# Kernel tuning notes

Hardware: AMD Instinct MI355X
Metric: run time of the kernel (lower is better)

## Reference

```python
import jax, jax.numpy as jnp
import numpy as np
from jax import lax

N_NODES = 50000
N_EDGES = 1_600_000
BATCH = 4
T_STEPS = 50
DT = 0.02  # integration step (s)


def setup_inputs() -> dict:
    key = jax.random.key(0)
    ks = jax.random.split(key, 8)
    x = jax.random.normal(ks[0], (BATCH, T_STEPS, N_NODES), jnp.float32) * 0.5
    # NeuronBias: normal(mean=0.5, std=0.05)
    bias = (jax.random.normal(ks[1], (N_NODES,), jnp.float32) * 0.05 + 0.5)
    # NeuronTimeConst: around 0.05s, kept positive
    time_const = jax.random.uniform(ks[2], (N_NODES,), jnp.float32) * 0.045 + 0.005
    # EdgeSign: +/-1
    sign = jnp.where(jax.random.uniform(ks[3], (N_EDGES,)) < 0.5, -1.0, 1.0).astype(jnp.float32)
    # SynCount: lognormal, non-negative
    syn_count = jnp.exp(jax.random.normal(ks[4], (N_EDGES,), jnp.float32) * 0.5)
    # SynStrength: small positive scale (scale_chem/scale_elec = 0.01)
    syn_strength = jax.random.uniform(ks[5], (N_EDGES,), jnp.float32) * 0.01
    src_idx = jax.random.randint(ks[6], (N_EDGES,), 0, N_NODES, dtype=jnp.int32)
    tgt_idx = jax.random.randint(ks[7], (N_EDGES,), 0, N_NODES, dtype=jnp.int32)
    return dict(x=x, bias=bias, time_const=time_const, sign=sign,
                syn_count=syn_count, syn_strength=syn_strength,
                src_idx=src_idx, tgt_idx=tgt_idx)


def reference(x, bias, time_const, sign, syn_count, syn_strength, src_idx, tgt_idx):
    """Recurrent connectome dynamics (StaticSynapses, relu activation).

    Per step: gather relu(v) at source nodes, weight each edge by
    sign*syn_count*syn_strength, scatter-add into target nodes, then Euler
    update v += dt/tau * (-v + bias + synaptic_input + stimulus).
    Returns relu(v) over time: [B, T, N].
    """
    B, T, N = x.shape
    # clamp configs: non_negative on counts/strengths
    weight = sign * jax.nn.relu(syn_count) * jax.nn.relu(syn_strength)  # [E]
    tau = jnp.maximum(time_const, DT)
    alpha = DT / tau  # [N]

    v0 = jnp.broadcast_to(bias, (B, N))  # initial state at bias

    def step(v, x_t):
        rates = jax.nn.relu(v)                      # [B, N]
        msg = rates[:, src_idx] * weight            # gather -> edge transform [B, E]
        summed = jnp.zeros((B, N), x.dtype).at[:, tgt_idx].add(msg)  # scatter-reduce
        v_new = v + alpha * (-v + bias + summed + x_t)
        return v_new, jax.nn.relu(v_new)

    _, out = lax.scan(step, v0, jnp.moveaxis(x, 1, 0))  # scan over T
    return jnp.moveaxis(out, 0, 1)  # [B, T, N]
```

## Files before the change

### kernel.cpp

```cpp
#include <hip/hip_runtime.h>
#include <hip/hip_fp16.h>

#define N_NODES 50000
#define N_EDGES 1600000
#define T_STEPS 50
#define DT      0.02f
#define NB      256
#define NPB     196
#define CAP     6912
#define TILE    4096
#define G       8


__global__ __launch_bounds__(256) void zero_kernel(int* __restrict__ bucket_count) {
    bucket_count[threadIdx.x] = 0;
}

__global__ __launch_bounds__(256) void init_kernel(
    const float* __restrict__ bias, const float* __restrict__ time_const,
    float* __restrict__ alpha, float* __restrict__ v ,
    float4* __restrict__ rates0)
{
    int n = blockIdx.x * 256 + threadIdx.x;
    if (n >= N_NODES) return;
    float tau = fmaxf(time_const[n], DT);
    alpha[n] = DT / tau;
    float b = bias[n];
    v[n] = b; v[N_NODES + n] = b; v[2 * N_NODES + n] = b; v[3 * N_NODES + n] = b;
    float r = fmaxf(b, 0.0f);
    rates0[n] = make_float4(r, r, r, r);
}

__global__ __launch_bounds__(256) void bucket_kernel(
    const int* __restrict__ src, const int* __restrict__ tgt,
    const float* __restrict__ sign, const float* __restrict__ syn_count,
    const float* __restrict__ syn_strength,
    int* __restrict__ bucket_count, unsigned long long* __restrict__ rec_buf)
{
    __shared__ int hist[NB], base_s[NB], cur[NB];
    int tid = threadIdx.x;
    hist[tid] = 0;
    __syncthreads();

    int e0 = blockIdx.x * TILE + tid;
    int bkt[16];
    unsigned long long item[16];
#pragma unroll
    for (int k = 0; k < 16; ++k) {
        int e = e0 + k * 256;
        if (e < N_EDGES) {
            int t = tgt[e];
            int b = t / NPB;
            int tl = t - b * NPB;
            float w = sign[e] * fmaxf(syn_count[e], 0.f) * fmaxf(syn_strength[e], 0.f);
            unsigned int rec = (unsigned int)src[e] |
                               ((unsigned int)__half_as_ushort(__float2half(w)) << 16);
            bkt[k] = b;
            item[k] = (unsigned long long)rec | ((unsigned long long)tl << 32);
            atomicAdd(&hist[b], 1);
        } else {
            bkt[k] = -1;
        }
    }
    __syncthreads();
    base_s[tid] = atomicAdd(&bucket_count[tid], hist[tid]);
    cur[tid] = 0;
    __syncthreads();
#pragma unroll
    for (int k = 0; k < 16; ++k) {
        if (bkt[k] >= 0) {
            int p = base_s[bkt[k]] + atomicAdd(&cur[bkt[k]], 1);
            if (p < CAP) rec_buf[(size_t)bkt[k] * CAP + p] = item[k];
        }
    }
}

__global__ __launch_bounds__(256) void sort_kernel(
    const int* __restrict__ bucket_count,
    const unsigned long long* __restrict__ rec_buf,
    unsigned int* __restrict__ edges_g, int* __restrict__ offsets)
{
    __shared__ unsigned int sorted[CAP];
    __shared__ int cnts[NB];
    __shared__ int loc_off[NPB + 1];
    __shared__ int loc_cur[NPB];

    int b = blockIdx.x;
    int tid = threadIdx.x;
    int node_base = b * NPB;
    int n_nodes = min(NPB, N_NODES - node_base);

    cnts[tid] = min(bucket_count[tid], CAP);
    if (tid < NPB) loc_cur[tid] = 0;
    __syncthreads();

    __shared__ int ebase_s;
    if (tid == 0) {
        int r = 0;
        for (int i = 0; i < b; ++i) r += cnts[i];
        ebase_s = r;
    }
    __syncthreads();
    int ebase = ebase_s;
    int cnt = cnts[b];

    for (int i = tid; i < cnt; i += 256) {
        unsigned long long it = rec_buf[(size_t)b * CAP + i];
        atomicAdd(&loc_cur[(int)(it >> 32)], 1);
    }
    __syncthreads();
    if (tid == 0) {
        int r = 0;
        for (int n = 0; n < n_nodes; ++n) { loc_off[n] = r; r += loc_cur[n]; }
        loc_off[n_nodes] = r;
    }
    __syncthreads();
    if (tid < n_nodes) loc_cur[tid] = loc_off[tid];
    __syncthreads();

    for (int i = tid; i < cnt; i += 256) {
        unsigned long long it = rec_buf[(size_t)b * CAP + i];
        int p = atomicAdd(&loc_cur[(int)(it >> 32)], 1);
        sorted[p] = (unsigned int)it;
    }
    __syncthreads();

    for (int i = tid; i < cnt; i += 256) edges_g[ebase + i] = sorted[i];
    for (int n = tid; n < n_nodes; n += 256) offsets[node_base + n] = ebase + loc_off[n];
    if (b == NB - 1 && tid == 0) offsets[N_NODES] = ebase + cnt;
}

__device__ __forceinline__ float rec_w(unsigned int rec) {
    return __half2float(__ushort_as_half((unsigned short)(rec >> 16)));
}

__global__ __launch_bounds__(256) void step_kernel(
    const float4* __restrict__ rates_in, float* __restrict__ rates_out,
    float* __restrict__ v ,
    const float* __restrict__ alpha, const float* __restrict__ bias,
    const int* __restrict__ offsets, const unsigned int* __restrict__ edges,
    const float* __restrict__ x, float* __restrict__ out, int t, int nblk)
{
    int nb8 = nblk / 8;
    int idx = blockIdx.x;
    int node_block = (idx < nb8 * 8) ? (idx % 8) * nb8 + idx / 8 : idx;
    int node = node_block * (256 / G) + ((int)threadIdx.x / G);
    int lane = threadIdx.x & (G - 1);
    if (node >= N_NODES) return;

    int beg = offsets[node], end = offsets[node + 1];
    float4 acc = make_float4(0.f, 0.f, 0.f, 0.f);

    int i = beg + lane;
    unsigned int r0 = (i          < end) ? edges[i]         : 0u;
    unsigned int r1 = (i + G      < end) ? edges[i + G]     : 0u;
    unsigned int r2 = (i + 2 * G  < end) ? edges[i + 2 * G] : 0u;
    unsigned int r3 = (i + 3 * G  < end) ? edges[i + 3 * G] : 0u;
    while (i < end) {
        unsigned int n0 = (i + 4 * G < end) ? edges[i + 4 * G] : 0u;
        unsigned int n1 = (i + 5 * G < end) ? edges[i + 5 * G] : 0u;
        unsigned int n2 = (i + 6 * G < end) ? edges[i + 6 * G] : 0u;
        unsigned int n3 = (i + 7 * G < end) ? edges[i + 7 * G] : 0u;
        float4 a0 = rates_in[r0 & 0xFFFFu];
        float4 a1 = rates_in[r1 & 0xFFFFu];
        float4 a2 = rates_in[r2 & 0xFFFFu];
        float4 a3 = rates_in[r3 & 0xFFFFu];
        float w0 = rec_w(r0), w1 = rec_w(r1), w2 = rec_w(r2), w3 = rec_w(r3);
        acc.x = fmaf(a0.x, w0, acc.x); acc.y = fmaf(a0.y, w0, acc.y);
        acc.z = fmaf(a0.z, w0, acc.z); acc.w = fmaf(a0.w, w0, acc.w);
        acc.x = fmaf(a1.x, w1, acc.x); acc.y = fmaf(a1.y, w1, acc.y);
        acc.z = fmaf(a1.z, w1, acc.z); acc.w = fmaf(a1.w, w1, acc.w);
        acc.x = fmaf(a2.x, w2, acc.x); acc.y = fmaf(a2.y, w2, acc.y);
        acc.z = fmaf(a2.z, w2, acc.z); acc.w = fmaf(a2.w, w2, acc.w);
        acc.x = fmaf(a3.x, w3, acc.x); acc.y = fmaf(a3.y, w3, acc.y);
        acc.z = fmaf(a3.z, w3, acc.z); acc.w = fmaf(a3.w, w3, acc.w);
        r0 = n0; r1 = n1; r2 = n2; r3 = n3;
        i += 4 * G;
    }

#pragma unroll
    for (int m = 1; m < G; m <<= 1) {
        acc.x += __shfl_xor(acc.x, m, 64);
        acc.y += __shfl_xor(acc.y, m, 64);
        acc.z += __shfl_xor(acc.z, m, 64);
        acc.w += __shfl_xor(acc.w, m, 64);
    }

    if (lane < 4) {
        float sum = (lane == 0) ? acc.x : (lane == 1) ? acc.y
                  : (lane == 2) ? acc.z : acc.w;
        float a = alpha[node];
        float b = bias[node];
        const int TN = T_STEPS * N_NODES;
        int vi = lane * N_NODES + node;
        int oi = lane * TN + t * N_NODES + node;
        float vv = v[vi];
        float vn = vv + a * (b + sum + x[oi] - vv);
        v[vi] = vn;
        float r = fmaxf(vn, 0.f);
        rates_out[node * 4 + lane] = r;
        out[oi] = r;
    }
}


extern "C" void kernel_launch(void* const* d_in, const int* in_sizes, int n_in,
                              void* d_out, int out_size, void* d_ws, size_t ws_size,
                              hipStream_t stream) {
    const float* x            = (const float*)d_in[0];
    const float* bias         = (const float*)d_in[1];
    const float* time_const   = (const float*)d_in[2];
    const float* sign         = (const float*)d_in[3];
    const float* syn_count    = (const float*)d_in[4];
    const float* syn_strength = (const float*)d_in[5];
    const int*   src_idx      = (const int*)d_in[6];
    const int*   tgt_idx      = (const int*)d_in[7];
    float* out = (float*)d_out;

    char* ws = (char*)d_ws;
    size_t off = 0;
    auto alloc = [&](size_t bytes) -> void* {
        void* p = ws + off;
        off = (off + bytes + 255) & ~(size_t)255;
        return p;
    };
    float* v        = (float*)alloc((size_t)N_NODES * 4 * 4);
    float* rates_a  = (float*)alloc((size_t)N_NODES * 16);
    float* rates_b  = (float*)alloc((size_t)N_NODES * 16);
    float* alpha    = (float*)alloc((size_t)N_NODES * 4);
    int*   offsets  = (int*)  alloc((size_t)(N_NODES + 1) * 4);
    int*   bucket_count = (int*)alloc((size_t)NB * 4);
    unsigned int* edges = (unsigned int*)alloc((size_t)N_EDGES * 4);
    unsigned long long* rec_buf =
        (unsigned long long*)alloc((size_t)NB * CAP * 8);

    int nb_nodes = (N_NODES + 255) / 256;
    int nb_tiles = (N_EDGES + TILE - 1) / TILE;

    zero_kernel<<<1, 256, 0, stream>>>(bucket_count);
    init_kernel<<<nb_nodes, 256, 0, stream>>>(bias, time_const, alpha, v,
                                              (float4*)rates_a);
    bucket_kernel<<<nb_tiles, 256, 0, stream>>>(src_idx, tgt_idx, sign, syn_count,
                                                syn_strength, bucket_count, rec_buf);
    sort_kernel<<<NB, 256, 0, stream>>>(bucket_count, rec_buf, edges, offsets);

    int nblk = (N_NODES + (256 / G) - 1) / (256 / G);
    for (int t = 0; t < T_STEPS; ++t) {
        const float4* rin  = (const float4*)((t & 1) ? rates_b : rates_a);
        float*        rout = (t & 1) ? rates_a : rates_b;
        step_kernel<<<nblk, 256, 0, stream>>>(rin, rout, v, alpha, bias,
                                              offsets, edges, x, out, t, nblk);
    }
}
```

Before: 735.8 us.

## Store rates in fp16, pad edge lists for paired loads, fuse init into sort

The per-node rate buffer is now stored as four fp16 values (8 bytes) instead of float4, which halves the bytes moved by each gathered edge read. Edge segments are padded to even length in fixed per-bucket slots, so each lane loads two edge records at once with a uint2 load. Explicit end offsets are stored per node. The init kernel is folded into the sort kernel, alpha and bias are packed into one float2, and nontemporal loads and stores are used for x and the output. Storing rates in fp16 adds rounding error to the recurrent state feeding each step.

```diff
diff --git a/kernel.cpp b/kernel.cpp
--- a/kernel.cpp
+++ b/kernel.cpp
@@ -8,27 +8,13 @@
 #define NB      256
 #define NPB     196
 #define CAP     6912
+#define CAP2    7168
 #define TILE    4096
 #define G       8
 
 
 __global__ __launch_bounds__(256) void zero_kernel(int* __restrict__ bucket_count) {
     bucket_count[threadIdx.x] = 0;
-}
-
-__global__ __launch_bounds__(256) void init_kernel(
-    const float* __restrict__ bias, const float* __restrict__ time_const,
-    float* __restrict__ alpha, float* __restrict__ v ,
-    float4* __restrict__ rates0)
-{
-    int n = blockIdx.x * 256 + threadIdx.x;
-    if (n >= N_NODES) return;
-    float tau = fmaxf(time_const[n], DT);
-    alpha[n] = DT / tau;
-    float b = bias[n];
-    v[n] = b; v[N_NODES + n] = b; v[2 * N_NODES + n] = b; v[3 * N_NODES + n] = b;
-    float r = fmaxf(b, 0.0f);
-    rates0[n] = make_float4(r, r, r, r);
 }
 
 __global__ __launch_bounds__(256) void bucket_kernel(
@@ -78,40 +64,39 @@
 __global__ __launch_bounds__(256) void sort_kernel(
     const int* __restrict__ bucket_count,
     const unsigned long long* __restrict__ rec_buf,
-    unsigned int* __restrict__ edges_g, int* __restrict__ offsets)
+    const float* __restrict__ bias, const float* __restrict__ time_const,
+    unsigned int* __restrict__ edges_g,
+    int* __restrict__ offsets, int* __restrict__ ends,
+    float2* __restrict__ ab, float* __restrict__ v ,
+    uint2* __restrict__ rates0 )
 {
-    __shared__ unsigned int sorted[CAP];
-    __shared__ int cnts[NB];
+    __shared__ unsigned int sorted[CAP2];
     __shared__ int loc_off[NPB + 1];
+    __shared__ int loc_cnt[NPB];
     __shared__ int loc_cur[NPB];
 
     int b = blockIdx.x;
     int tid = threadIdx.x;
     int node_base = b * NPB;
     int n_nodes = min(NPB, N_NODES - node_base);
-
-    cnts[tid] = min(bucket_count[tid], CAP);
-    if (tid < NPB) loc_cur[tid] = 0;
-    __syncthreads();
-
-    __shared__ int ebase_s;
+    int ebase = b * CAP2;
+    int cnt = min(bucket_count[b], CAP);
+
+    for (int i = tid; i < CAP2; i += 256) sorted[i] = 0;
+    if (tid < NPB) loc_cnt[tid] = 0;
+    __syncthreads();
+
+    for (int i = tid; i < cnt; i += 256) {
+        unsigned long long it = rec_buf[(size_t)b * CAP + i];
+        atomicAdd(&loc_cnt[(int)(it >> 32)], 1);
+    }
+    __syncthreads();
     if (tid == 0) {
         int r = 0;
-        for (int i = 0; i < b; ++i) r += cnts[i];
-        ebase_s = r;
-    }
-    __syncthreads();
-    int ebase = ebase_s;
-    int cnt = cnts[b];
-
-    for (int i = tid; i < cnt; i += 256) {
-        unsigned long long it = rec_buf[(size_t)b * CAP + i];
-        atomicAdd(&loc_cur[(int)(it >> 32)], 1);
-    }
-    __syncthreads();
-    if (tid == 0) {
-        int r = 0;
-        for (int n = 0; n < n_nodes; ++n) { loc_off[n] = r; r += loc_cur[n]; }
+        for (int n = 0; n < n_nodes; ++n) {
+            loc_off[n] = r;
+            r += (loc_cnt[n] + 1) & ~1;
+        }
         loc_off[n_nodes] = r;
     }
     __syncthreads();
@@ -125,20 +110,42 @@
     }
     __syncthreads();
 
-    for (int i = tid; i < cnt; i += 256) edges_g[ebase + i] = sorted[i];
-    for (int n = tid; n < n_nodes; n += 256) offsets[node_base + n] = ebase + loc_off[n];
-    if (b == NB - 1 && tid == 0) offsets[N_NODES] = ebase + cnt;
+    int total = loc_off[n_nodes];
+    for (int i = tid; i < total; i += 256) edges_g[ebase + i] = sorted[i];
+    for (int n = tid; n < n_nodes; n += 256) {
+        int gn = node_base + n;
+        offsets[gn] = ebase + loc_off[n];
+        ends[gn]    = ebase + loc_off[n + 1];
+        float bb  = bias[gn];
+        float tau = fmaxf(time_const[gn], DT);
+        ab[gn] = make_float2(DT / tau, bb);
+        v[gn] = bb; v[N_NODES + gn] = bb;
+        v[2 * N_NODES + gn] = bb; v[3 * N_NODES + gn] = bb;
+        __half hr = __float2half(fmaxf(bb, 0.f));
+        __half2 h2 = __halves2half2(hr, hr);
+        uint2 r0; r0.x = *(unsigned int*)&h2; r0.y = r0.x;
+        rates0[gn] = r0;
+    }
 }
 
 __device__ __forceinline__ float rec_w(unsigned int rec) {
     return __half2float(__ushort_as_half((unsigned short)(rec >> 16)));
 }
+__device__ __forceinline__ float4 h4_to_f4(uint2 g) {
+    __half2 h01 = *(__half2*)&g.x;
+    __half2 h23 = *(__half2*)&g.y;
+    float2 f01 = __half22float2(h01);
+    float2 f23 = __half22float2(h23);
+    return make_float4(f01.x, f01.y, f23.x, f23.y);
+}
 
 __global__ __launch_bounds__(256) void step_kernel(
-    const float4* __restrict__ rates_in, float* __restrict__ rates_out,
+    const uint2* __restrict__ rates_in ,
+    __half* __restrict__ rates_out ,
     float* __restrict__ v ,
-    const float* __restrict__ alpha, const float* __restrict__ bias,
-    const int* __restrict__ offsets, const unsigned int* __restrict__ edges,
+    const float2* __restrict__ ab,
+    const int* __restrict__ offsets, const int* __restrict__ ends,
+    const unsigned int* __restrict__ edges,
     const float* __restrict__ x, float* __restrict__ out, int t, int nblk)
 {
     int nb8 = nblk / 8;
@@ -148,24 +155,21 @@
     int lane = threadIdx.x & (G - 1);
     if (node >= N_NODES) return;
 
-    int beg = offsets[node], end = offsets[node + 1];
+    int beg = offsets[node], end = ends[node];
     float4 acc = make_float4(0.f, 0.f, 0.f, 0.f);
 
-    int i = beg + lane;
-    unsigned int r0 = (i          < end) ? edges[i]         : 0u;
-    unsigned int r1 = (i + G      < end) ? edges[i + G]     : 0u;
-    unsigned int r2 = (i + 2 * G  < end) ? edges[i + 2 * G] : 0u;
-    unsigned int r3 = (i + 3 * G  < end) ? edges[i + 3 * G] : 0u;
+    const uint2 zz = make_uint2(0u, 0u);
+    int i = beg + 2 * lane;
+    uint2 p0 = (i          < end) ? *(const uint2*)(edges + i)          : zz;
+    uint2 p1 = (i + 2 * G  < end) ? *(const uint2*)(edges + i + 2 * G)  : zz;
     while (i < end) {
-        unsigned int n0 = (i + 4 * G < end) ? edges[i + 4 * G] : 0u;
-        unsigned int n1 = (i + 5 * G < end) ? edges[i + 5 * G] : 0u;
-        unsigned int n2 = (i + 6 * G < end) ? edges[i + 6 * G] : 0u;
-        unsigned int n3 = (i + 7 * G < end) ? edges[i + 7 * G] : 0u;
-        float4 a0 = rates_in[r0 & 0xFFFFu];
-        float4 a1 = rates_in[r1 & 0xFFFFu];
-        float4 a2 = rates_in[r2 & 0xFFFFu];
-        float4 a3 = rates_in[r3 & 0xFFFFu];
-        float w0 = rec_w(r0), w1 = rec_w(r1), w2 = rec_w(r2), w3 = rec_w(r3);
+        uint2 q0 = (i + 4 * G < end) ? *(const uint2*)(edges + i + 4 * G) : zz;
+        uint2 q1 = (i + 6 * G < end) ? *(const uint2*)(edges + i + 6 * G) : zz;
+        float4 a0 = h4_to_f4(rates_in[p0.x & 0xFFFFu]);
+        float4 a1 = h4_to_f4(rates_in[p0.y & 0xFFFFu]);
+        float4 a2 = h4_to_f4(rates_in[p1.x & 0xFFFFu]);
+        float4 a3 = h4_to_f4(rates_in[p1.y & 0xFFFFu]);
+        float w0 = rec_w(p0.x), w1 = rec_w(p0.y), w2 = rec_w(p1.x), w3 = rec_w(p1.y);
         acc.x = fmaf(a0.x, w0, acc.x); acc.y = fmaf(a0.y, w0, acc.y);
         acc.z = fmaf(a0.z, w0, acc.z); acc.w = fmaf(a0.w, w0, acc.w);
         acc.x = fmaf(a1.x, w1, acc.x); acc.y = fmaf(a1.y, w1, acc.y);
@@ -174,7 +178,7 @@
         acc.z = fmaf(a2.z, w2, acc.z); acc.w = fmaf(a2.w, w2, acc.w);
         acc.x = fmaf(a3.x, w3, acc.x); acc.y = fmaf(a3.y, w3, acc.y);
         acc.z = fmaf(a3.z, w3, acc.z); acc.w = fmaf(a3.w, w3, acc.w);
-        r0 = n0; r1 = n1; r2 = n2; r3 = n3;
+        p0 = q0; p1 = q1;
         i += 4 * G;
     }
 
@@ -189,17 +193,17 @@
     if (lane < 4) {
         float sum = (lane == 0) ? acc.x : (lane == 1) ? acc.y
                   : (lane == 2) ? acc.z : acc.w;
-        float a = alpha[node];
-        float b = bias[node];
+        float2 abv = ab[node];
         const int TN = T_STEPS * N_NODES;
         int vi = lane * N_NODES + node;
         int oi = lane * TN + t * N_NODES + node;
         float vv = v[vi];
-        float vn = vv + a * (b + sum + x[oi] - vv);
+        float xv = __builtin_nontemporal_load(x + oi);
+        float vn = vv + abv.x * (abv.y + sum + xv - vv);
         v[vi] = vn;
         float r = fmaxf(vn, 0.f);
-        rates_out[node * 4 + lane] = r;
-        out[oi] = r;
+        rates_out[node * 4 + lane] = __float2half(r);
+        __builtin_nontemporal_store(r, out + oi);
     }
 }
 
@@ -224,31 +228,30 @@
         off = (off + bytes + 255) & ~(size_t)255;
         return p;
     };
-    float* v        = (float*)alloc((size_t)N_NODES * 4 * 4);
-    float* rates_a  = (float*)alloc((size_t)N_NODES * 16);
-    float* rates_b  = (float*)alloc((size_t)N_NODES * 16);
-    float* alpha    = (float*)alloc((size_t)N_NODES * 4);
-    int*   offsets  = (int*)  alloc((size_t)(N_NODES + 1) * 4);
-    int*   bucket_count = (int*)alloc((size_t)NB * 4);
-    unsigned int* edges = (unsigned int*)alloc((size_t)N_EDGES * 4);
+    float*  v       = (float*) alloc((size_t)N_NODES * 4 * 4);
+    uint2*  rates_a = (uint2*) alloc((size_t)N_NODES * 8);
+    uint2*  rates_b = (uint2*) alloc((size_t)N_NODES * 8);
+    float2* ab      = (float2*)alloc((size_t)N_NODES * 8);
+    int*    offsets = (int*)   alloc((size_t)N_NODES * 4);
+    int*    ends    = (int*)   alloc((size_t)N_NODES * 4);
+    int*    bucket_count = (int*)alloc((size_t)NB * 4);
+    unsigned int* edges = (unsigned int*)alloc((size_t)NB * CAP2 * 4);
     unsigned long long* rec_buf =
         (unsigned long long*)alloc((size_t)NB * CAP * 8);
 
-    int nb_nodes = (N_NODES + 255) / 256;
     int nb_tiles = (N_EDGES + TILE - 1) / TILE;
 
     zero_kernel<<<1, 256, 0, stream>>>(bucket_count);
-    init_kernel<<<nb_nodes, 256, 0, stream>>>(bias, time_const, alpha, v,
-                                              (float4*)rates_a);
     bucket_kernel<<<nb_tiles, 256, 0, stream>>>(src_idx, tgt_idx, sign, syn_count,
                                                 syn_strength, bucket_count, rec_buf);
-    sort_kernel<<<NB, 256, 0, stream>>>(bucket_count, rec_buf, edges, offsets);
+    sort_kernel<<<NB, 256, 0, stream>>>(bucket_count, rec_buf, bias, time_const,
+                                        edges, offsets, ends, ab, v, rates_a);
 
     int nblk = (N_NODES + (256 / G) - 1) / (256 / G);
     for (int t = 0; t < T_STEPS; ++t) {
-        const float4* rin  = (const float4*)((t & 1) ? rates_b : rates_a);
-        float*        rout = (t & 1) ? rates_a : rates_b;
-        step_kernel<<<nblk, 256, 0, stream>>>(rin, rout, v, alpha, bias,
-                                              offsets, edges, x, out, t, nblk);
-    }
-}
+        const uint2* rin  = (t & 1) ? rates_b : rates_a;
+        __half*      rout = (__half*)((t & 1) ? rates_a : rates_b);
+        step_kernel<<<nblk, 256, 0, stream>>>(rin, rout, v, ab,
+                                              offsets, ends, edges, x, out, t, nblk);
+    }
+}
```

Result: slower. 788.9 us (+7.2%).
